# Kernel optimization log

Hardware: AMD Instinct MI355X
Metric: run time of the kernel (lower is better)

## Reference

```python
import jax, jax.numpy as jnp
import numpy as np

B, V, M, H, L, T = 4, 2048, 8192, 64, 5, 4


def setup_inputs() -> dict:
    key = jax.random.key(0)
    ks = jax.random.split(key, 24)
    inp = {
        "input_llr": jax.random.normal(ks[0], (B, V), jnp.float32),
        "message_to_var_mapping": jax.random.randint(ks[1], (M,), 0, V, jnp.int32),
        "message_types": jax.random.randint(ks[2], (M,), 0, T, jnp.int32),
        "var_to_check_adjacency": jax.random.uniform(ks[3], (M, M), jnp.float32),
        "check_to_var_adjacency": jax.random.uniform(ks[4], (M, M), jnp.float32),
    }
    s = 0.05
    # input_embedding: Linear(1, H)
    inp["w_in"] = jax.random.normal(ks[5], (H,), jnp.float32) * s
    inp["b_in"] = jax.random.normal(ks[6], (H,), jnp.float32) * s
    # per-layer params, stacked over L iterations
    inp["type_emb"] = jax.random.normal(ks[7], (L, T, H), jnp.float32) * s
    inp["w1v"] = jax.random.normal(ks[8], (L, 2 * H, H), jnp.float32) * s
    inp["b1v"] = jax.random.normal(ks[9], (L, H), jnp.float32) * s
    inp["w2v"] = jax.random.normal(ks[10], (L, H, H), jnp.float32) * s
    inp["b2v"] = jax.random.normal(ks[11], (L, H), jnp.float32) * s
    inp["w1c"] = jax.random.normal(ks[12], (L, 2 * H, H), jnp.float32) * s
    inp["b1c"] = jax.random.normal(ks[13], (L, H), jnp.float32) * s
    inp["w2c"] = jax.random.normal(ks[14], (L, H, H), jnp.float32) * s
    inp["b2c"] = jax.random.normal(ks[15], (L, H), jnp.float32) * s
    # output_projection of the LAST gnn layer (the one used by decode_messages)
    inp["proj_w"] = jax.random.normal(ks[16], (H,), jnp.float32) * s
    inp["proj_b"] = jax.random.normal(ks[17], (), jnp.float32) * s
    return inp


def reference(input_llr, message_to_var_mapping, message_types,
              var_to_check_adjacency, check_to_var_adjacency,
              w_in, b_in, type_emb, w1v, b1v, w2v, b2v,
              w1c, b1c, w2c, b2c, proj_w, proj_b):
    Bv, Vn = input_llr.shape
    # gather message LLRs from variable nodes: (B, M)
    msg_llr = input_llr[:, message_to_var_mapping]
    # input embedding Linear(1, H): (B, M, H)
    feat = msg_llr[..., None] * w_in + b_in
    safe_types = jnp.clip(message_types, 0, T - 1)
    n_layers = type_emb.shape[0]
    for i in range(n_layers):
        te = type_emb[i][safe_types]                      # (M, H)
        comb = feat + te                                  # (B, M, H)
        v2c = jnp.einsum('mn,bnh->bmh', var_to_check_adjacency, comb)
        uv = jnp.concatenate([comb, v2c], axis=-1)        # (B, M, 2H)
        uv = jax.nn.relu(uv @ w1v[i] + b1v[i]) @ w2v[i] + b2v[i]
        c2v = jnp.einsum('mn,bnh->bmh', check_to_var_adjacency, comb)
        uc = jnp.concatenate([comb, c2v], axis=-1)
        uc = jax.nn.relu(uc @ w1c[i] + b1c[i]) @ w2c[i] + b2c[i]
        upd = uv + uc
        if i > 0:  # residual applied only after first iteration (per source)
            upd = upd + feat
        feat = upd
    # decode with last layer's output projection: (B, M)
    decoded = feat @ proj_w + proj_b
    # sum-aggregate message LLRs back to variable nodes: (B, V)
    var_llrs = jax.ops.segment_sum(decoded.T, message_to_var_mapping,
                                   num_segments=Vn).T
    return jax.nn.sigmoid(var_llrs + input_llr)
```

## Files before the change

kernel.cpp:

```cpp
#include <hip/hip_runtime.h>
#include <math.h>

static constexpr int CB = 4;
static constexpr int CV = 2048;
static constexpr int CM = 8192;
static constexpr int CH = 64;
static constexpr int CL = 5;
static constexpr int CT = 4;
static constexpr int RR = CM * CB;
static constexpr int WCAT_STRIDE = 192 * 128 + 128 * 64 + 128 + 64;

typedef float f32x4 __attribute__((ext_vector_type(4)));
typedef short bf16x8 __attribute__((ext_vector_type(8)));
typedef unsigned int u32;
typedef unsigned short u16;

__device__ inline u16 f2bf(float x) {
    u32 u = __float_as_uint(x);
    u += 0x7FFF + ((u >> 16) & 1);
    return (u16)(u >> 16);
}
__device__ inline float bf2f(u16 b) { return __uint_as_float(((u32)b) << 16); }

#define GLOAD16(gp, lp)                                                         \
    __builtin_amdgcn_global_load_lds(                                           \
        (const __attribute__((address_space(1))) unsigned int*)(gp),            \
        (__attribute__((address_space(3))) unsigned int*)(lp), 16, 0, 0)

__global__ void k_init_feat(const float* __restrict__ llr, const int* __restrict__ map,
                            const float* __restrict__ w_in, const float* __restrict__ b_in,
                            float* __restrict__ feat) {
    int idx = blockIdx.x * blockDim.x + threadIdx.x;
    int h = idx & 63;
    int r = idx >> 6;
    int m = r >> 2;
    int b = r & 3;
    float v = llr[b * CV + map[m]];
    feat[idx] = v * w_in[h] + b_in[h];
}

__global__ void k_comb(const float* __restrict__ feat, const int* __restrict__ types,
                       const float* __restrict__ te, float* __restrict__ in2) {
    int idx = blockIdx.x * blockDim.x + threadIdx.x;
    int h = idx & 63;
    int r = idx >> 6;
    int m = r >> 2;
    int t = types[m];
    t = t < 0 ? 0 : (t > CT - 1 ? CT - 1 : t);
    in2[(size_t)r * 192 + h] = feat[idx] + te[t * CH + h];
}

__global__ void k_splitA(const float* __restrict__ Avc, const float* __restrict__ Acv,
                         u16* __restrict__ Aprep) {
    size_t t = (size_t)blockIdx.x * 256 + threadIdx.x;
    int lane = (int)(t & 63);
    int rf = (int)((t >> 6) & 511);
    int ki4 = (int)((t >> 15) & 63);
    int adj = (int)(t >> 21);
    const float* __restrict__ A = adj ? Acv : Avc;
    int r = rf * 16 + (lane & 15);
    const float* rp = A + (size_t)r * CM + ki4 * 128 + (lane >> 4) * 8;
    float4 v0[4], v1[4];
#pragma unroll
    for (int u = 0; u < 4; ++u) {
        v0[u] = *(const float4*)(rp + u * 32);
        v1[u] = *(const float4*)(rp + u * 32 + 4);
    }
#pragma unroll
    for (int u = 0; u < 4; ++u) {
        float vv[8] = {v0[u].x, v0[u].y, v0[u].z, v0[u].w,
                       v1[u].x, v1[u].y, v1[u].z, v1[u].w};
        u32 hw[4], lw[4];
#pragma unroll
        for (int j = 0; j < 4; ++j) {
            float a0 = vv[2 * j], a1 = vv[2 * j + 1];
            u16 h0 = f2bf(a0), h1 = f2bf(a1);
            u16 g0 = f2bf(a0 - bf2f(h0)), g1 = f2bf(a1 - bf2f(h1));
            hw[j] = (u32)h0 | ((u32)h1 << 16);
            lw[j] = (u32)g0 | ((u32)g1 << 16);
        }
        u16* dp = Aprep + ((((size_t)adj * 256 + ki4 * 4 + u) * 512) + rf) * 1024 + lane * 8;
        *(uint4*)dp = make_uint4(hw[0], hw[1], hw[2], hw[3]);
        *(uint4*)(dp + 512) = make_uint4(lw[0], lw[1], lw[2], lw[3]);
    }
}

__global__ void k_transposeB(const float* __restrict__ feat, const int* __restrict__ types,
                             const float* __restrict__ te, char* __restrict__ BprepC,
                             float* __restrict__ in2) {
    __shared__ float tile[64][65];
    __shared__ float teL[4][64];
    __shared__ int ty[64];
    const int tid = threadIdx.x;
    const int m0 = blockIdx.x * 64;
    teL[tid >> 6][tid & 63] = te[tid];
    if (tid < 64) {
        int tt = types[m0 + tid];
        ty[tid] = tt < 0 ? 0 : (tt > CT - 1 ? CT - 1 : tt);
    }
    __syncthreads();
    for (int b = 0; b < 4; ++b) {
        __syncthreads();
        {
            const int mr = tid >> 2, hc = (tid & 3) * 16;
            const float* fp = feat + ((size_t)(m0 + mr) * 4 + b) * 64 + hc;
            float* op = in2 + ((size_t)(m0 + mr) * 4 + b) * 192 + hc;
            const int tt = ty[mr];
#pragma unroll
            for (int j = 0; j < 4; ++j) {
                float4 v = *(const float4*)(fp + j * 4);
                float4 c;
                c.x = v.x + teL[tt][hc + j * 4 + 0];
                c.y = v.y + teL[tt][hc + j * 4 + 1];
                c.z = v.z + teL[tt][hc + j * 4 + 2];
                c.w = v.w + teL[tt][hc + j * 4 + 3];
                tile[mr][hc + j * 4 + 0] = c.x;
                tile[mr][hc + j * 4 + 1] = c.y;
                tile[mr][hc + j * 4 + 2] = c.z;
                tile[mr][hc + j * 4 + 3] = c.w;
                *(float4*)(op + j * 4) = c;
            }
        }
        __syncthreads();
        {
            const int h = tid & 63, mg = tid >> 6;
            u32 hw[8], lw[8];
#pragma unroll
            for (int q = 0; q < 8; ++q) {
                float v0 = tile[mg * 16 + 2 * q + 0][h];
                float v1 = tile[mg * 16 + 2 * q + 1][h];
                u16 h0 = f2bf(v0), h1 = f2bf(v1);
                u16 g0 = f2bf(v0 - bf2f(h0)), g1 = f2bf(v1 - bf2f(h1));
                hw[q] = (u32)h0 | ((u32)h1 << 16);
                lw[q] = (u32)g0 | ((u32)g1 << 16);
            }
            const int c = b * 64 + h;
            const int mstart = m0 + mg * 16;
            const int ki = mstart >> 5;
            const int q0 = (mstart >> 3) & 3;
            const int swzc = (c & 7) << 4;
            char* rowp = BprepC + (size_t)ki * 32768 + c * 128;
            *(uint4*)(rowp + (((q0 + 0) * 16) ^ swzc)) = make_uint4(hw[0], hw[1], hw[2], hw[3]);
            *(uint4*)(rowp + (((q0 + 1) * 16) ^ swzc)) = make_uint4(hw[4], hw[5], hw[6], hw[7]);
            *(uint4*)(rowp + (((4 + q0) * 16) ^ swzc)) = make_uint4(lw[0], lw[1], lw[2], lw[3]);
            *(uint4*)(rowp + (((5 + q0) * 16) ^ swzc)) = make_uint4(lw[4], lw[5], lw[6], lw[7]);
        }
    }
}

__global__ __launch_bounds__(512, 1) void k_adjmfma_fast(
    const char* __restrict__ AprepC, const char* __restrict__ BprepC,
    float* __restrict__ pbuf) {
    __shared__ char frames[2][49152];

    int lin = blockIdx.y * 64 + blockIdx.x;
    lin = (lin & 7) * 32 + (lin >> 3);
    const int bx = lin & 63;
    const int by = lin >> 6;
    const int adj = by >> 1;
    const int ks = by & 1;

    const int tid = threadIdx.x;
    const int lane = tid & 63;
    const int wid = tid >> 6;
    const int wr = wid >> 2;
    const int wc = wid & 3;
    const int l15 = lane & 15, l4 = lane >> 4;
    const int m0 = bx * 128;

    const size_t abase = (((size_t)adj * 256) * 512 + (size_t)bx * 8) * 2048;

#define STAGE(F, S)                                                              \
    {                                                                            \
        int ki_ = ks * 128 + (S); if (ki_ > 255) ki_ = 255;                      \
        const char* as_ = AprepC + abase + (size_t)ki_ * (512 * 2048);           \
        char* fr_ = &frames[F][0];                                               \
        GLOAD16(as_ + tid * 16, fr_ + tid * 16);                                 \
        GLOAD16(as_ + 8192 + tid * 16, fr_ + 8192 + tid * 16);                   \
        const char* bs_ = BprepC + ((size_t)ki_ << 15);                          \
        GLOAD16(bs_ + tid * 16, fr_ + 16384 + tid * 16);                         \
        GLOAD16(bs_ + 8192 + tid * 16, fr_ + 24576 + tid * 16);                  \
        GLOAD16(bs_ + 16384 + tid * 16, fr_ + 32768 + tid * 16);                 \
        GLOAD16(bs_ + 24576 + tid * 16, fr_ + 40960 + tid * 16);                 \
    }

    f32x4 acc[4][4] = {};

    STAGE(0, 0);
    STAGE(1, 1);

#pragma unroll 2
    for (int s = 0; s < 128; ++s) {
        const int f = s & 1;
        asm volatile("s_waitcnt vmcnt(6)" ::: "memory");
        asm volatile("s_barrier" ::: "memory");
        const char* fr = &frames[f][0];
        bf16x8 bh[4], bl[4];
#pragma unroll
        for (int nf = 0; nf < 4; ++nf) {
            const int col = wc * 64 + nf * 16 + l15;
            const char* rb = fr + 16384 + col * 128;
            const int swz = (col & 7) << 4;
            bh[nf] = *(const bf16x8*)(rb + ((l4 * 16) ^ swz));
            bl[nf] = *(const bf16x8*)(rb + (((4 + l4) * 16) ^ swz));
        }
#pragma unroll
        for (int mf = 0; mf < 4; ++mf) {
            const char* ra = fr + (wr * 4 + mf) * 2048 + lane * 16;
            bf16x8 ah = *(const bf16x8*)ra;
            bf16x8 al = *(const bf16x8*)(ra + 1024);
#pragma unroll
            for (int nf = 0; nf < 4; ++nf) {
                acc[mf][nf] = __builtin_amdgcn_mfma_f32_16x16x32_bf16(ah, bh[nf], acc[mf][nf], 0, 0, 0);
                acc[mf][nf] = __builtin_amdgcn_mfma_f32_16x16x32_bf16(ah, bl[nf], acc[mf][nf], 0, 0, 0);
                acc[mf][nf] = __builtin_amdgcn_mfma_f32_16x16x32_bf16(al, bh[nf], acc[mf][nf], 0, 0, 0);
            }
        }
        asm volatile("s_barrier" ::: "memory");
        STAGE(f, s + 2);
    }
    asm volatile("s_waitcnt vmcnt(0)" ::: "memory");

    float* pb = pbuf + (size_t)by * ((size_t)CM * 256);
#pragma unroll
    for (int mf = 0; mf < 4; ++mf) {
#pragma unroll
        for (int nf = 0; nf < 4; ++nf) {
            const int col = wc * 64 + nf * 16 + l15;
#pragma unroll
            for (int r = 0; r < 4; ++r) {
                const int m = m0 + wr * 64 + mf * 16 + l4 * 4 + r;
                pb[(size_t)m * 256 + col] = acc[mf][nf][r];
            }
        }
    }
#undef STAGE
}

__global__ void k_transpose(const float* __restrict__ feat, const int* __restrict__ types,
                            const float* __restrict__ te,
                            u16* __restrict__ BH, u16* __restrict__ BL) {
    __shared__ float tile[64][65];
    __shared__ float teL[4][64];
    __shared__ int ty[64];
    const int tid = threadIdx.x;
    const int m0 = blockIdx.x * 64;
    teL[tid >> 6][tid & 63] = te[tid];
    if (tid < 64) {
        int t = types[m0 + tid];
        ty[tid] = t < 0 ? 0 : (t > CT - 1 ? CT - 1 : t);
    }
    __syncthreads();
    for (int b = 0; b < 4; ++b) {
        __syncthreads();
        {
            const int mr = tid >> 2, hc = (tid & 3) * 16;
            const float* fp = feat + ((size_t)(m0 + mr) * 4 + b) * 64 + hc;
            const int t = ty[mr];
#pragma unroll
            for (int j = 0; j < 4; ++j) {
                float4 v = *(const float4*)(fp + j * 4);
                tile[mr][hc + j * 4 + 0] = v.x + teL[t][hc + j * 4 + 0];
                tile[mr][hc + j * 4 + 1] = v.y + teL[t][hc + j * 4 + 1];
                tile[mr][hc + j * 4 + 2] = v.z + teL[t][hc + j * 4 + 2];
                tile[mr][hc + j * 4 + 3] = v.w + teL[t][hc + j * 4 + 3];
            }
        }
        __syncthreads();
        {
            const int h = tid & 63, mg = tid >> 6;
            u32 hw[8], lw[8];
#pragma unroll
            for (int q = 0; q < 8; ++q) {
                float v0 = tile[mg * 16 + 2 * q + 0][h];
                float v1 = tile[mg * 16 + 2 * q + 1][h];
                u16 h0 = f2bf(v0), h1 = f2bf(v1);
                u16 g0 = f2bf(v0 - bf2f(h0)), g1 = f2bf(v1 - bf2f(h1));
                hw[q] = (u32)h0 | ((u32)h1 << 16);
                lw[q] = (u32)g0 | ((u32)g1 << 16);
            }
            size_t obase = (size_t)(b * 64 + h) * CM + m0 + mg * 16;
            *(uint4*)(BH + obase) = make_uint4(hw[0], hw[1], hw[2], hw[3]);
            *(uint4*)(BH + obase + 8) = make_uint4(hw[4], hw[5], hw[6], hw[7]);
            *(uint4*)(BL + obase) = make_uint4(lw[0], lw[1], lw[2], lw[3]);
            *(uint4*)(BL + obase + 8) = make_uint4(lw[4], lw[5], lw[6], lw[7]);
        }
    }
}

__global__ __launch_bounds__(512, 2) void k_adjmfma_fb(
    const float* __restrict__ A0, const float* __restrict__ A1,
    const u16* __restrict__ BH, const u16* __restrict__ BL,
    float* __restrict__ pbuf) {
    __shared__ char lA[128 * 128];
    __shared__ char lB[256 * 128];

    const int tid = threadIdx.x;
    const int adj = blockIdx.y >> 1;
    const int ks = blockIdx.y & 1;
    const int m0 = blockIdx.x * 128;
    const float* __restrict__ A = adj ? A1 : A0;
    const int kbase = ks * 4096;

    const int lane = tid & 63;
    const int wid = tid >> 6;
    const int wr = wid >> 2;
    const int wc = wid & 3;
    const int l15 = lane & 15, l4 = lane >> 4;

    const int sa_row = tid >> 2, sa_kq = tid & 3;
    const int sb_col = tid >> 1, sb_part = tid & 1;

    f32x4 acc[4][4] = {};

    for (int k0 = 0; k0 < 4096; k0 += 32) {
        {
            const float* ap = A + (size_t)(m0 + sa_row) * CM + kbase + k0 + sa_kq * 8;
            float4 v0 = *(const float4*)ap;
            float4 v1 = *(const float4*)(ap + 4);
            float vv[8] = {v0.x, v0.y, v0.z, v0.w, v1.x, v1.y, v1.z, v1.w};
            u32 hw[4], lw[4];
#pragma unroll
            for (int j = 0; j < 4; ++j) {
                float a0 = vv[2 * j], a1 = vv[2 * j + 1];
                u16 h0 = f2bf(a0), h1 = f2bf(a1);
                u16 g0 = f2bf(a0 - bf2f(h0)), g1 = f2bf(a1 - bf2f(h1));
                hw[j] = (u32)h0 | ((u32)h1 << 16);
                lw[j] = (u32)g0 | ((u32)g1 << 16);
            }
            char* base = lA + sa_row * 128;
            const int swz = (sa_row & 7) << 4;
            *(uint4*)(base + ((sa_kq * 16) ^ swz)) = make_uint4(hw[0], hw[1], hw[2], hw[3]);
            *(uint4*)(base + ((64 + sa_kq * 16) ^ swz)) = make_uint4(lw[0], lw[1], lw[2], lw[3]);
        }
        {
            const u16* src = (sb_part ? BL : BH) + (size_t)sb_col * CM + kbase + k0;
            char* base = lB + sb_col * 128;
            const int swz = (sb_col & 7) << 4;
            const int lb = sb_part * 64;
#pragma unroll
            for (int j = 0; j < 4; ++j) {
                uint4 v = *(const uint4*)(src + j * 8);
                *(uint4*)(base + ((lb + j * 16) ^ swz)) = v;
            }
        }
        __syncthreads();

        bf16x8 bh[4], bl[4];
#pragma unroll
        for (int nf = 0; nf < 4; ++nf) {
            const int col = wc * 64 + nf * 16 + l15;
            const char* rb = lB + col * 128;
            const int swz = (col & 7) << 4;
            bh[nf] = *(const bf16x8*)(rb + ((l4 * 16) ^ swz));
            bl[nf] = *(const bf16x8*)(rb + ((64 + l4 * 16) ^ swz));
        }
#pragma unroll
        for (int mf = 0; mf < 4; ++mf) {
            const int row = wr * 64 + mf * 16 + l15;
            const char* ra = lA + row * 128;
            const int swz = (row & 7) << 4;
            bf16x8 ah = *(const bf16x8*)(ra + ((l4 * 16) ^ swz));
            bf16x8 al = *(const bf16x8*)(ra + ((64 + l4 * 16) ^ swz));
#pragma unroll
            for (int nf = 0; nf < 4; ++nf) {
                acc[mf][nf] = __builtin_amdgcn_mfma_f32_16x16x32_bf16(ah, bh[nf], acc[mf][nf], 0, 0, 0);
                acc[mf][nf] = __builtin_amdgcn_mfma_f32_16x16x32_bf16(ah, bl[nf], acc[mf][nf], 0, 0, 0);
                acc[mf][nf] = __builtin_amdgcn_mfma_f32_16x16x32_bf16(al, bh[nf], acc[mf][nf], 0, 0, 0);
            }
        }
        __syncthreads();
    }

    float* pb = pbuf + (size_t)blockIdx.y * ((size_t)CM * 256);
#pragma unroll
    for (int mf = 0; mf < 4; ++mf) {
#pragma unroll
        for (int nf = 0; nf < 4; ++nf) {
            const int col = wc * 64 + nf * 16 + l15;
#pragma unroll
            for (int r = 0; r < 4; ++r) {
                const int m = m0 + wr * 64 + mf * 16 + l4 * 4 + r;
                pb[(size_t)m * 256 + col] = acc[mf][nf][r];
            }
        }
    }
}

__global__ void k_reduce(const float* __restrict__ pbuf, float* __restrict__ in2) {
    int idx = blockIdx.x * blockDim.x + threadIdx.x;
    int adj = idx >> 19;
    int rem = idx & ((1 << 19) - 1);
    int m = rem >> 6;
    int f4 = rem & 63;
    size_t o = (size_t)m * 256 + (size_t)f4 * 4;
    const float* p0 = pbuf + (size_t)(adj * 2) * ((size_t)CM * 256);
    const float* p1 = p0 + (size_t)CM * 256;
    float4 a = *(const float4*)(p0 + o);
    float4 b4 = *(const float4*)(p1 + o);
    a.x += b4.x; a.y += b4.y; a.z += b4.z; a.w += b4.w;
    int col = f4 * 4;
    int bb = col >> 6, h = col & 63;
    *(float4*)&in2[((size_t)m * 4 + bb) * 192 + 64 + adj * 64 + h] = a;
}

__global__ void k_prep(const float* __restrict__ w1v, const float* __restrict__ b1v,
                       const float* __restrict__ w2v, const float* __restrict__ b2v,
                       const float* __restrict__ w1c, const float* __restrict__ b1c,
                       const float* __restrict__ w2c, const float* __restrict__ b2c,
                       float* __restrict__ wcat) {
    int idx = blockIdx.x * blockDim.x + threadIdx.x;
    int total = CL * WCAT_STRIDE;
    if (idx >= total) return;
    int i = idx / WCAT_STRIDE;
    int e = idx % WCAT_STRIDE;
    float v;
    if (e < 24576) {
        int j = e >> 7, k = e & 127;
        if (j < 64)        v = (k < 64) ? w1v[(i * 128 + j) * 64 + k]
                                        : w1c[(i * 128 + j) * 64 + (k - 64)];
        else if (j < 128)  v = (k < 64) ? w1v[(i * 128 + j) * 64 + k] : 0.f;
        else               v = (k < 64) ? 0.f : w1c[(i * 128 + (j - 64)) * 64 + (k - 64)];
    } else if (e < 32768) {
        int e2 = e - 24576; int k = e2 >> 6, h = e2 & 63;
        v = (k < 64) ? w2v[(i * 64 + k) * 64 + h]
                     : w2c[(i * 64 + (k - 64)) * 64 + h];
    } else if (e < 32896) {
        int k = e - 32768;
        v = (k < 64) ? b1v[i * 64 + k] : b1c[i * 64 + (k - 64)];
    } else {
        int h = e - 32896;
        v = b2v[i * 64 + h] + b2c[i * 64 + h];
    }
    wcat[idx] = v;
}

template<int OMODE, int RES>
__global__ __launch_bounds__(256) void k_gemm(
    const float* __restrict__ A0, int lda,
    const float* __restrict__ Bm, int ldb,
    float* __restrict__ O, const float* __restrict__ bias,
    const float* __restrict__ resid, int K) {
    __shared__ float As[32][64];
    __shared__ float Bs[32][68];

    const int tid = threadIdx.x;
    const int m0 = blockIdx.y * 64;
    const int c0 = blockIdx.x * 64;
    const int tm = (tid & 15) * 4;
    const int tn = (tid >> 4) * 4;
    const int arow = tid & 63;
    const int akg = (tid >> 6) * 8;
    const int bk = tid >> 4;
    const int bc = (tid & 15) * 4;

    float acc[4][4] = {};

    for (int k0 = 0; k0 < K; k0 += 32) {
        const float* Ap = A0 + (size_t)(m0 + arow) * (size_t)lda + k0 + akg;
        float4 a0 = *(const float4*)Ap;
        float4 a1 = *(const float4*)(Ap + 4);
        float4 b0 = *(const float4*)(Bm + (size_t)(k0 + bk) * (size_t)ldb + c0 + bc);
        float4 b1 = *(const float4*)(Bm + (size_t)(k0 + bk + 16) * (size_t)ldb + c0 + bc);
        As[akg + 0][arow] = a0.x;
        As[akg + 1][arow] = a0.y;
        As[akg + 2][arow] = a0.z;
        As[akg + 3][arow] = a0.w;
        As[akg + 4][arow] = a1.x;
        As[akg + 5][arow] = a1.y;
        As[akg + 6][arow] = a1.z;
        As[akg + 7][arow] = a1.w;
        *(float4*)&Bs[bk][bc] = b0;
        *(float4*)&Bs[bk + 16][bc] = b1;
        __syncthreads();
#pragma unroll
        for (int k = 0; k < 32; ++k) {
            float4 av = *(const float4*)&As[k][tm];
            float4 bv = *(const float4*)&Bs[k][tn];
            float a_[4] = {av.x, av.y, av.z, av.w};
            float b_[4] = {bv.x, bv.y, bv.z, bv.w};
#pragma unroll
            for (int i = 0; i < 4; ++i)
#pragma unroll
                for (int j = 0; j < 4; ++j)
                    acc[i][j] = fmaf(a_[i], b_[j], acc[i][j]);
        }
        __syncthreads();
    }

#pragma unroll
    for (int i = 0; i < 4; ++i) {
        int m = m0 + tm + i;
        float4 x = make_float4(acc[i][0], acc[i][1], acc[i][2], acc[i][3]);
        if (OMODE == 1) {
            const float4 bv = *(const float4*)&bias[c0 + tn];
            x.x = fmaxf(x.x + bv.x, 0.f);
            x.y = fmaxf(x.y + bv.y, 0.f);
            x.z = fmaxf(x.z + bv.z, 0.f);
            x.w = fmaxf(x.w + bv.w, 0.f);
            *(float4*)&O[(size_t)m * 128 + c0 + tn] = x;
        } else {
            const float4 bv = *(const float4*)&bias[tn];
            x.x += bv.x; x.y += bv.y; x.z += bv.z; x.w += bv.w;
            if (RES) {
                const float4 rv = *(const float4*)&resid[(size_t)m * 64 + tn];
                x.x += rv.x; x.y += rv.y; x.z += rv.z; x.w += rv.w;
            }
            *(float4*)&O[(size_t)m * 64 + tn] = x;
        }
    }
}

__global__ void k_zero(float* __restrict__ p, int n) {
    int i = blockIdx.x * blockDim.x + threadIdx.x;
    if (i < n) p[i] = 0.f;
}

__global__ void k_decode(const float* __restrict__ feat, const float* __restrict__ proj_w,
                         const float* __restrict__ proj_b, const int* __restrict__ map,
                         float* __restrict__ var_llrs) {
    int r = blockIdx.x * 4 + (threadIdx.x >> 6);
    int lane = threadIdx.x & 63;
    float v = feat[(size_t)r * 64 + lane] * proj_w[lane];
#pragma unroll
    for (int off = 32; off > 0; off >>= 1) v += __shfl_down(v, off);
    if (lane == 0) {
        int m = r >> 2, b = r & 3;
        atomicAdd(&var_llrs[b * CV + map[m]], v + proj_b[0]);
    }
}

__global__ void k_final(const float* __restrict__ var_llrs, const float* __restrict__ llr,
                        float* __restrict__ out) {
    int i = blockIdx.x * blockDim.x + threadIdx.x;
    float x = var_llrs[i] + llr[i];
    out[i] = 1.f / (1.f + expf(-x));
}

extern "C" void kernel_launch(void* const* d_in, const int* in_sizes, int n_in,
                              void* d_out, int out_size, void* d_ws, size_t ws_size,
                              hipStream_t stream) {
    const float* llr   = (const float*)d_in[0];
    const int*   map   = (const int*)d_in[1];
    const int*   types = (const int*)d_in[2];
    const float* Avc   = (const float*)d_in[3];
    const float* Acv   = (const float*)d_in[4];
    const float* w_in  = (const float*)d_in[5];
    const float* b_in  = (const float*)d_in[6];
    const float* temb  = (const float*)d_in[7];
    const float* w1v   = (const float*)d_in[8];
    const float* b1v   = (const float*)d_in[9];
    const float* w2v   = (const float*)d_in[10];
    const float* b2v   = (const float*)d_in[11];
    const float* w1c   = (const float*)d_in[12];
    const float* b1c   = (const float*)d_in[13];
    const float* w2c   = (const float*)d_in[14];
    const float* b2c   = (const float*)d_in[15];
    const float* projw = (const float*)d_in[16];
    const float* projb = (const float*)d_in[17];
    float* out = (float*)d_out;

    constexpr size_t OFF_FEAT = 0;
    constexpr size_t OFF_IN2  = OFF_FEAT + (size_t)RR * 64 * 4;
    constexpr size_t OFF_HID  = OFF_IN2 + (size_t)RR * 192 * 4;
    constexpr size_t OFF_WCAT = OFF_HID + (size_t)RR * 128 * 4;
    constexpr size_t OFF_VLLR = OFF_WCAT + (size_t)CL * WCAT_STRIDE * 4;
    constexpr size_t OFF_PBUF = OFF_VLLR + 8192 * 4;
    constexpr size_t OFF_X    = OFF_PBUF + (size_t)4 * CM * 256 * 4;
    constexpr size_t BPREP_BYTES = (size_t)256 * 256 * 128 + 32768;
    constexpr size_t OFF_APREP   = OFF_X + BPREP_BYTES;
    constexpr size_t APREP_BYTES = (size_t)2 * 256 * 512 * 2048 + 8192;
    constexpr size_t NEED_FAST   = OFF_APREP + APREP_BYTES;
    constexpr size_t OFF_CTH = OFF_X;
    constexpr size_t OFF_CTL = OFF_CTH + (size_t)256 * CM * 2;

    char* ws = (char*)d_ws;
    float* feat = (float*)(ws + OFF_FEAT);
    float* in2  = (float*)(ws + OFF_IN2);
    float* hid  = (float*)(ws + OFF_HID);
    float* wcat = (float*)(ws + OFF_WCAT);
    float* vllr = (float*)(ws + OFF_VLLR);
    float* pbuf = (float*)(ws + OFF_PBUF);

    const bool fast = ws_size >= NEED_FAST;

    k_zero<<<(CB * CV + 255) / 256, 256, 0, stream>>>(vllr, CB * CV);
    k_prep<<<(CL * WCAT_STRIDE + 255) / 256, 256, 0, stream>>>(
        w1v, b1v, w2v, b2v, w1c, b1c, w2c, b2c, wcat);
    k_init_feat<<<(RR * CH) / 256, 256, 0, stream>>>(llr, map, w_in, b_in, feat);

    u16* Aprep = (u16*)(ws + OFF_APREP);
    char* Bprep = ws + OFF_X;
    u16* combTH = (u16*)(ws + OFF_CTH);
    u16* combTL = (u16*)(ws + OFF_CTL);

    if (fast)
        k_splitA<<<16384, 256, 0, stream>>>(Avc, Acv, Aprep);

    for (int i = 0; i < CL; ++i) {
        float* wc = wcat + (size_t)i * WCAT_STRIDE;
        const float* te = temb + i * CT * CH;
        if (fast) {
            k_transposeB<<<CM / 64, 256, 0, stream>>>(feat, types, te, Bprep, in2);
            k_adjmfma_fast<<<dim3(64, 4), 512, 0, stream>>>((const char*)Aprep, Bprep, pbuf);
        } else {
            k_comb<<<(RR * CH) / 256, 256, 0, stream>>>(feat, types, te, in2);
            k_transpose<<<CM / 64, 256, 0, stream>>>(feat, types, te, combTH, combTL);
            k_adjmfma_fb<<<dim3(64, 4), 512, 0, stream>>>(Avc, Acv, combTH, combTL, pbuf);
        }
        k_reduce<<<(2 * CM * 64) / 256, 256, 0, stream>>>(pbuf, in2);
        k_gemm<1, 0><<<dim3(2, 512), 256, 0, stream>>>(
            in2, 192, wc, 128, hid, wc + 32768, nullptr, 192);
        if (i == 0)
            k_gemm<2, 0><<<dim3(1, 512), 256, 0, stream>>>(
                hid, 128, wc + 24576, 64, feat, wc + 32896, feat, 128);
        else
            k_gemm<2, 1><<<dim3(1, 512), 256, 0, stream>>>(
                hid, 128, wc + 24576, 64, feat, wc + 32896, feat, 128);
    }

    k_decode<<<RR / 4, 256, 0, stream>>>(feat, projw, projb, map, vllr);
    k_final<<<(CB * CV) / 256, 256, 0, stream>>>(vllr, llr, out);
}
```

Baseline: 1.363 ms.

## Fuse split-K reduce into first MLP GEMM, triple-buffer adjacency MFMA, LDS-stage splitA

Adds k_gemm1f, which reads the comb activations and sums the two split-K partial buffers from pbuf while loading its A tile. This removes the separate k_reduce kernel and the write of a 192-wide in2 concatenation. The adjacency MFMA kernel now uses three LDS frames so two stages are in flight instead of one, at the cost of more shared memory. k_splitA stages a 16x512 tile through shared memory so that global reads and writes are coalesced.

```diff
diff --git a/kernel.cpp b/kernel.cpp
--- a/kernel.cpp
+++ b/kernel.cpp
@@ -50,44 +50,58 @@
     in2[(size_t)r * 192 + h] = feat[idx] + te[t * CH + h];
 }
 
-__global__ void k_splitA(const float* __restrict__ Avc, const float* __restrict__ Acv,
-                         u16* __restrict__ Aprep) {
-    size_t t = (size_t)blockIdx.x * 256 + threadIdx.x;
-    int lane = (int)(t & 63);
-    int rf = (int)((t >> 6) & 511);
-    int ki4 = (int)((t >> 15) & 63);
-    int adj = (int)(t >> 21);
+__global__ __launch_bounds__(256) void k_splitA(const float* __restrict__ Avc,
+                                                const float* __restrict__ Acv,
+                                                u16* __restrict__ Aprep) {
+    __shared__ float lds[16][516];
+    const int blk = blockIdx.x;
+    const int adj = blk >> 13;
+    const int rem = blk & 8191;
+    const int rf = rem & 511;
+    const int kig = rem >> 9;
     const float* __restrict__ A = adj ? Acv : Avc;
-    int r = rf * 16 + (lane & 15);
-    const float* rp = A + (size_t)r * CM + ki4 * 128 + (lane >> 4) * 8;
-    float4 v0[4], v1[4];
-#pragma unroll
-    for (int u = 0; u < 4; ++u) {
-        v0[u] = *(const float4*)(rp + u * 32);
-        v1[u] = *(const float4*)(rp + u * 32 + 4);
-    }
-#pragma unroll
-    for (int u = 0; u < 4; ++u) {
-        float vv[8] = {v0[u].x, v0[u].y, v0[u].z, v0[u].w,
-                       v1[u].x, v1[u].y, v1[u].z, v1[u].w};
-        u32 hw[4], lw[4];
-#pragma unroll
-        for (int j = 0; j < 4; ++j) {
-            float a0 = vv[2 * j], a1 = vv[2 * j + 1];
-            u16 h0 = f2bf(a0), h1 = f2bf(a1);
-            u16 g0 = f2bf(a0 - bf2f(h0)), g1 = f2bf(a1 - bf2f(h1));
-            hw[j] = (u32)h0 | ((u32)h1 << 16);
-            lw[j] = (u32)g0 | ((u32)g1 << 16);
-        }
-        u16* dp = Aprep + ((((size_t)adj * 256 + ki4 * 4 + u) * 512) + rf) * 1024 + lane * 8;
-        *(uint4*)dp = make_uint4(hw[0], hw[1], hw[2], hw[3]);
-        *(uint4*)(dp + 512) = make_uint4(lw[0], lw[1], lw[2], lw[3]);
+    const int t = threadIdx.x;
+    {
+        const int rl = t >> 4, cc = t & 15;
+        const float* rp = A + (size_t)(rf * 16 + rl) * CM + kig * 512 + cc * 32;
+#pragma unroll
+        for (int j = 0; j < 8; ++j) {
+            float4 v = *(const float4*)(rp + j * 4);
+            *(float4*)&lds[rl][cc * 32 + j * 4] = v;
+        }
+    }
+    __syncthreads();
+    {
+        const int r = t & 15, kl = t >> 4;
+        float e[32];
+#pragma unroll
+        for (int j = 0; j < 8; ++j) {
+            float4 v = *(const float4*)&lds[r][kl * 32 + j * 4];
+            e[j * 4 + 0] = v.x; e[j * 4 + 1] = v.y;
+            e[j * 4 + 2] = v.z; e[j * 4 + 3] = v.w;
+        }
+        const size_t base = (((size_t)adj * 256 + kig * 16 + kl) * 512 + rf) * 1024;
+#pragma unroll
+        for (int c = 0; c < 4; ++c) {
+            u32 hw[4], lw[4];
+#pragma unroll
+            for (int j = 0; j < 4; ++j) {
+                float a0 = e[c * 8 + 2 * j], a1 = e[c * 8 + 2 * j + 1];
+                u16 h0 = f2bf(a0), h1 = f2bf(a1);
+                u16 g0 = f2bf(a0 - bf2f(h0)), g1 = f2bf(a1 - bf2f(h1));
+                hw[j] = (u32)h0 | ((u32)h1 << 16);
+                lw[j] = (u32)g0 | ((u32)g1 << 16);
+            }
+            u16* dp = Aprep + base + (size_t)(r + 16 * c) * 8;
+            *(uint4*)dp = make_uint4(hw[0], hw[1], hw[2], hw[3]);
+            *(uint4*)(dp + 512) = make_uint4(lw[0], lw[1], lw[2], lw[3]);
+        }
     }
 }
 
 __global__ void k_transposeB(const float* __restrict__ feat, const int* __restrict__ types,
                              const float* __restrict__ te, char* __restrict__ BprepC,
-                             float* __restrict__ in2) {
+                             float* __restrict__ comb) {
     __shared__ float tile[64][65];
     __shared__ float teL[4][64];
     __shared__ int ty[64];
@@ -104,7 +118,7 @@
         {
             const int mr = tid >> 2, hc = (tid & 3) * 16;
             const float* fp = feat + ((size_t)(m0 + mr) * 4 + b) * 64 + hc;
-            float* op = in2 + ((size_t)(m0 + mr) * 4 + b) * 192 + hc;
+            float* op = comb + ((size_t)(m0 + mr) * 4 + b) * 64 + hc;
             const int tt = ty[mr];
 #pragma unroll
             for (int j = 0; j < 4; ++j) {
@@ -151,7 +165,7 @@
 __global__ __launch_bounds__(512, 1) void k_adjmfma_fast(
     const char* __restrict__ AprepC, const char* __restrict__ BprepC,
     float* __restrict__ pbuf) {
-    __shared__ char frames[2][49152];
+    __shared__ char frames[3][49152];
 
     int lin = blockIdx.y * 64 + blockIdx.x;
     lin = (lin & 7) * 32 + (lin >> 3);
@@ -170,29 +184,28 @@
 
     const size_t abase = (((size_t)adj * 256) * 512 + (size_t)bx * 8) * 2048;
 
-#define STAGE(F, S)                                                              \
+#define STAGE3(FP, S)                                                            \
     {                                                                            \
         int ki_ = ks * 128 + (S); if (ki_ > 255) ki_ = 255;                      \
         const char* as_ = AprepC + abase + (size_t)ki_ * (512 * 2048);           \
-        char* fr_ = &frames[F][0];                                               \
-        GLOAD16(as_ + tid * 16, fr_ + tid * 16);                                 \
-        GLOAD16(as_ + 8192 + tid * 16, fr_ + 8192 + tid * 16);                   \
+        GLOAD16(as_ + tid * 16, (FP) + tid * 16);                                \
+        GLOAD16(as_ + 8192 + tid * 16, (FP) + 8192 + tid * 16);                  \
         const char* bs_ = BprepC + ((size_t)ki_ << 15);                          \
-        GLOAD16(bs_ + tid * 16, fr_ + 16384 + tid * 16);                         \
-        GLOAD16(bs_ + 8192 + tid * 16, fr_ + 24576 + tid * 16);                  \
-        GLOAD16(bs_ + 16384 + tid * 16, fr_ + 32768 + tid * 16);                 \
-        GLOAD16(bs_ + 24576 + tid * 16, fr_ + 40960 + tid * 16);                 \
+        GLOAD16(bs_ + tid * 16, (FP) + 16384 + tid * 16);                        \
+        GLOAD16(bs_ + 8192 + tid * 16, (FP) + 24576 + tid * 16);                 \
+        GLOAD16(bs_ + 16384 + tid * 16, (FP) + 32768 + tid * 16);                \
+        GLOAD16(bs_ + 24576 + tid * 16, (FP) + 40960 + tid * 16);                \
     }
 
     f32x4 acc[4][4] = {};
 
-    STAGE(0, 0);
-    STAGE(1, 1);
-
-#pragma unroll 2
+    STAGE3(&frames[0][0], 0);
+    STAGE3(&frames[1][0], 1);
+    STAGE3(&frames[2][0], 2);
+
+    int f = 0;
     for (int s = 0; s < 128; ++s) {
-        const int f = s & 1;
-        asm volatile("s_waitcnt vmcnt(6)" ::: "memory");
+        asm volatile("s_waitcnt vmcnt(12)" ::: "memory");
         asm volatile("s_barrier" ::: "memory");
         const char* fr = &frames[f][0];
         bf16x8 bh[4], bl[4];
@@ -217,7 +230,8 @@
             }
         }
         asm volatile("s_barrier" ::: "memory");
-        STAGE(f, s + 2);
+        STAGE3(fr, s + 3);
+        f = (f == 2) ? 0 : f + 1;
     }
     asm volatile("s_waitcnt vmcnt(0)" ::: "memory");
 
@@ -234,7 +248,87 @@
             }
         }
     }
-#undef STAGE
+#undef STAGE3
+}
+
+__global__ __launch_bounds__(256) void k_gemm1f(
+    const float* __restrict__ comb, const float* __restrict__ pbuf,
+    const float* __restrict__ wc, float* __restrict__ hid) {
+    __shared__ float As[32][64];
+    __shared__ float Bs[32][68];
+
+    const int tid = threadIdx.x;
+    const int m0 = blockIdx.y * 64;
+    const int c0 = blockIdx.x * 64;
+    const int tm = (tid & 15) * 4;
+    const int tn = (tid >> 4) * 4;
+    const int arow = tid & 63;
+    const int akg = (tid >> 6) * 8;
+    const int bk = tid >> 4;
+    const int bc = (tid & 15) * 4;
+    const float* bias = wc + 32768;
+
+    float acc[4][4] = {};
+
+    for (int k0 = 0; k0 < 192; k0 += 32) {
+        const int krow = k0 + akg;
+        const int r = m0 + arow;
+        float4 a0, a1;
+        if (krow < 64) {
+            const float* ap = comb + (size_t)r * 64 + krow;
+            a0 = *(const float4*)ap;
+            a1 = *(const float4*)(ap + 4);
+        } else {
+            const int adj = (krow - 64) >> 6;
+            const int h = (krow - 64) & 63;
+            const float* p = pbuf + (size_t)(adj * 2) * ((size_t)CM * 256)
+                           + (size_t)(r >> 2) * 256 + (r & 3) * 64 + h;
+            float4 x0 = *(const float4*)p;
+            float4 x1 = *(const float4*)(p + 4);
+            float4 y0 = *(const float4*)(p + (size_t)CM * 256);
+            float4 y1 = *(const float4*)(p + (size_t)CM * 256 + 4);
+            a0.x = x0.x + y0.x; a0.y = x0.y + y0.y; a0.z = x0.z + y0.z; a0.w = x0.w + y0.w;
+            a1.x = x1.x + y1.x; a1.y = x1.y + y1.y; a1.z = x1.z + y1.z; a1.w = x1.w + y1.w;
+        }
+        float4 b0 = *(const float4*)(wc + (size_t)(k0 + bk) * 128 + c0 + bc);
+        float4 b1 = *(const float4*)(wc + (size_t)(k0 + bk + 16) * 128 + c0 + bc);
+        As[akg + 0][arow] = a0.x;
+        As[akg + 1][arow] = a0.y;
+        As[akg + 2][arow] = a0.z;
+        As[akg + 3][arow] = a0.w;
+        As[akg + 4][arow] = a1.x;
+        As[akg + 5][arow] = a1.y;
+        As[akg + 6][arow] = a1.z;
+        As[akg + 7][arow] = a1.w;
+        *(float4*)&Bs[bk][bc] = b0;
+        *(float4*)&Bs[bk + 16][bc] = b1;
+        __syncthreads();
+#pragma unroll
+        for (int k = 0; k < 32; ++k) {
+            float4 av = *(const float4*)&As[k][tm];
+            float4 bv = *(const float4*)&Bs[k][tn];
+            float a_[4] = {av.x, av.y, av.z, av.w};
+            float b_[4] = {bv.x, bv.y, bv.z, bv.w};
+#pragma unroll
+            for (int i = 0; i < 4; ++i)
+#pragma unroll
+                for (int j = 0; j < 4; ++j)
+                    acc[i][j] = fmaf(a_[i], b_[j], acc[i][j]);
+        }
+        __syncthreads();
+    }
+
+#pragma unroll
+    for (int i = 0; i < 4; ++i) {
+        int m = m0 + tm + i;
+        float4 x = make_float4(acc[i][0], acc[i][1], acc[i][2], acc[i][3]);
+        const float4 bv = *(const float4*)&bias[c0 + tn];
+        x.x = fmaxf(x.x + bv.x, 0.f);
+        x.y = fmaxf(x.y + bv.y, 0.f);
+        x.z = fmaxf(x.z + bv.z, 0.f);
+        x.w = fmaxf(x.w + bv.w, 0.f);
+        *(float4*)&hid[(size_t)m * 128 + c0 + tn] = x;
+    }
 }
 
 __global__ void k_transpose(const float* __restrict__ feat, const int* __restrict__ types,
@@ -577,6 +671,7 @@
     char* ws = (char*)d_ws;
     float* feat = (float*)(ws + OFF_FEAT);
     float* in2  = (float*)(ws + OFF_IN2);
+    float* comb = (float*)(ws + OFF_IN2);
     float* hid  = (float*)(ws + OFF_HID);
     float* wcat = (float*)(ws + OFF_WCAT);
     float* vllr = (float*)(ws + OFF_VLLR);
@@ -601,16 +696,17 @@
         float* wc = wcat + (size_t)i * WCAT_STRIDE;
         const float* te = temb + i * CT * CH;
         if (fast) {
-            k_transposeB<<<CM / 64, 256, 0, stream>>>(feat, types, te, Bprep, in2);
+            k_transposeB<<<CM / 64, 256, 0, stream>>>(feat, types, te, Bprep, comb);
             k_adjmfma_fast<<<dim3(64, 4), 512, 0, stream>>>((const char*)Aprep, Bprep, pbuf);
+            k_gemm1f<<<dim3(2, 512), 256, 0, stream>>>(comb, pbuf, wc, hid);
         } else {
             k_comb<<<(RR * CH) / 256, 256, 0, stream>>>(feat, types, te, in2);
             k_transpose<<<CM / 64, 256, 0, stream>>>(feat, types, te, combTH, combTL);
             k_adjmfma_fb<<<dim3(64, 4), 512, 0, stream>>>(Avc, Acv, combTH, combTL, pbuf);
-        }
-        k_reduce<<<(2 * CM * 64) / 256, 256, 0, stream>>>(pbuf, in2);
-        k_gemm<1, 0><<<dim3(2, 512), 256, 0, stream>>>(
-            in2, 192, wc, 128, hid, wc + 32768, nullptr, 192);
+            k_reduce<<<(2 * CM * 64) / 256, 256, 0, stream>>>(pbuf, in2);
+            k_gemm<1, 0><<<dim3(2, 512), 256, 0, stream>>>(
+                in2, 192, wc, 128, hid, wc + 32768, nullptr, 192);
+        }
         if (i == 0)
             k_gemm<2, 0><<<dim3(1, 512), 256, 0, stream>>>(
                 hid, 128, wc + 24576, 64, feat, wc + 32896, feat, 128);
```

Measured after the change: 1.352 ms. No clear change (-0.9%).
